# Performance work log

Hardware: AMD Instinct MI355X
Metric: run time of the kernel (lower is better)

Reference implementation:

```python
import jax, jax.numpy as jnp
import numpy as np

B, T, V, D, NOPS = 4, 2048, 8192, 512, 8
HID = 2 * D  # ActionPolicy default hidden_dim
POL_OUT = D + NOPS + D


def setup_inputs() -> dict:
    key = jax.random.key(0)
    ks = jax.random.split(key, 12)
    std = 0.02
    x = jax.random.normal(ks[0], (B, T, V), dtype=jnp.float32)
    Wc = jax.random.normal(ks[1], (D, V), dtype=jnp.float32) * std   # compress (torch Linear weight: out,in)
    We = jax.random.normal(ks[2], (V, D), dtype=jnp.float32) * std   # expand
    Wq = jax.random.normal(ks[3], (D, D), dtype=jnp.float32) * std
    Wk = jax.random.normal(ks[4], (D, D), dtype=jnp.float32) * std
    Wv = jax.random.normal(ks[5], (D, D), dtype=jnp.float32) * std
    W1 = jax.random.normal(ks[6], (HID, D), dtype=jnp.float32) * std
    b1 = jnp.zeros((HID,), dtype=jnp.float32)
    W2 = jax.random.normal(ks[7], (POL_OUT, HID), dtype=jnp.float32) * std
    b2 = jnp.zeros((POL_OUT,), dtype=jnp.float32)
    Wops = jax.random.normal(ks[8], (NOPS, D, D), dtype=jnp.float32) * std  # 8 op-bank Linears (no bias)
    decay_logit = jnp.float32(3.0)
    mem_scale = jnp.float32(0.1)
    act_scale = jnp.float32(0.1)
    return {"x": x, "Wc": Wc, "We": We, "Wq": Wq, "Wk": Wk, "Wv": Wv,
            "W1": W1, "b1": b1, "W2": W2, "b2": b2, "Wops": Wops,
            "decay_logit": decay_logit, "mem_scale": mem_scale, "act_scale": act_scale}


_ACTS = [
    lambda h: jax.nn.gelu(h, approximate=False),
    jax.nn.relu,
    lambda h: jnp.square(jax.nn.relu(h)),
    jax.nn.silu,
    jnp.tanh,
    jax.nn.sigmoid,
    lambda h: h,
    lambda h: -h,
]


def reference(x, Wc, We, Wq, Wk, Wv, W1, b1, W2, b2, Wops,
              decay_logit, mem_scale, act_scale):
    d, k = D, NOPS
    # RMSNorm over vocab dim (torch F.rms_norm, eps = dtype eps by default)
    eps = jnp.asarray(jnp.finfo(x.dtype).eps, x.dtype)
    xn = x * jax.lax.rsqrt(jnp.mean(x * x, axis=-1, keepdims=True) + eps)
    h = xn @ Wc.T                                   # (B,T,d)

    # _cross_position: causal power-decay linear attention (no softmax)
    q = h @ Wq.T
    kk = h @ Wk.T
    v = h @ Wv.T
    scores = jnp.einsum('bid,bjd->bij', q, kk)      # (B,T,T)
    pos = jnp.arange(T)
    diff = pos[None, :] - pos[:, None]              # diff[i,j] = j - i
    decay = jax.nn.sigmoid(decay_logit)
    expo = jnp.maximum(diff - 1, 0).astype(x.dtype)
    w = jnp.power(decay, expo) * (diff > 0).astype(x.dtype)
    mem = jnp.einsum('bij,bjd->bid', scores * w[None], v)
    h = h + mem_scale * mem

    # ActionPolicy MLP
    pol = jax.nn.gelu(h @ W1.T + b1, approximate=False) @ W2.T + b2
    read_w = jax.nn.softmax(pol[..., :d], axis=-1)
    op_w = jax.nn.softmax(pol[..., d:d + k], axis=-1)
    write_w = jax.nn.sigmoid(pol[..., d + k:])

    # OpBank: soft-weighted mixture of 8 Linear+activation ops
    sel = h * read_w
    hs = jnp.einsum('btd,ned->nbte', sel, Wops)     # all 8 GEMMs batched
    transformed = jnp.zeros_like(sel)
    for i, act in enumerate(_ACTS):
        transformed = transformed + op_w[..., i:i + 1] * act(hs[i])

    result = transformed * write_w
    return (result @ We.T) * act_scale              # (B,T,V)
```

## Files before the change

kernel.cpp:

```cpp
#include <hip/hip_runtime.h>
#include <cmath>


namespace {

constexpr int Tt = 2048, Vv = 8192, Dd = 512, HID = 1024, PO = 1032;
constexpr int NTOK = 8192;

typedef unsigned short u16;
typedef u16 u16x4 __attribute__((ext_vector_type(4)));
typedef u16 u16x8 __attribute__((ext_vector_type(8)));
typedef short bf16x8 __attribute__((ext_vector_type(8)));
typedef float f32x4 __attribute__((ext_vector_type(4)));

enum { EPI_STORE_F32 = 0, EPI_STORE_P, EPI_VT_P, EPI_DECAY_P, EPI_ACCUM,
       EPI_GELU_P, EPI_BIAS_F32, EPI_OUT };

__device__ __forceinline__ u16 bf16_rn(float a) {
  union { float f; unsigned u; } c; c.f = a;
  return (u16)((c.u + 0x7FFFu + ((c.u >> 16) & 1u)) >> 16);
}
__device__ __forceinline__ void split2(float a, u16& hi, u16& lo) {
  const u16 h = bf16_rn(a);
  union { unsigned u; float f; } hf; hf.u = ((unsigned)h) << 16;
  hi = h; lo = bf16_rn(a - hf.f);
}
__device__ __forceinline__ int swz(int flat, int nwg) {
  const int xcd = flat & 7, pos = flat >> 3;
  const int q8 = nwg >> 3, r8 = nwg & 7;
  return (xcd < r8 ? xcd * (q8 + 1) : r8 * (q8 + 1) + (xcd - r8) * q8) + pos;
}

template <int EPI, bool AF32, bool SKIPK, bool NGUARD>
__launch_bounds__(256, 3)
__global__ void gemm_mfma(int gridX, int N, int K,
                          const void* __restrict__ Aptr, int lda, long long sAz, long long aPlane,
                          const u16* __restrict__ Bptr, int ldb, long long sBz, long long bPlane,
                          void* __restrict__ Cptr, int ldc, long long sCz, long long cPlane,
                          const float* __restrict__ rowScale,
                          const float* __restrict__ bias,
                          const float* __restrict__ scale_ptr,
                          const float* __restrict__ decayPow) {
  const int flat = swz(blockIdx.x, gridDim.x);
  const int bx = flat % gridX, by = flat / gridX, bz = blockIdx.z;
  if (EPI == EPI_DECAY_P && bx * 64 + 63 <= by * 128) return;

  __shared__ u16 AsH[128][40], AsL[128][40], BsH[64][40], BsL[64][40];
  const int tid = threadIdx.x;
  const int sr = tid >> 1, sc = (tid & 1) << 4;
  const int br = tid >> 2, bc = (tid & 3) << 3;
  const int arow = by * 128 + sr;
  const int brow = bx * 64 + br;
  const bool bok = !NGUARD || (brow < N);
  const int w = tid >> 6, lane = tid & 63;
  const int wr = (w >> 1) << 6, wc = (w & 1) << 5;
  const int r16 = lane & 15, kg = lane >> 4;

  float ascale = 1.0f;
  if (AF32 && rowScale) ascale = rowScale[arow];

  f32x4 acc[4][2];
#pragma unroll
  for (int i = 0; i < 4; ++i)
#pragma unroll
    for (int j = 0; j < 2; ++j) acc[i][j] = (f32x4)0.0f;

  const int k0 = SKIPK ? by * 128 : 0;

  float4 raf[4];
  u16x8 rah[2], ral[2], rbh, rbl;

  auto load_tiles = [&](int kt) {
    if constexpr (AF32) {
      const float* Aq = (const float*)Aptr + (long long)bz * sAz + (long long)arow * lda + kt + sc;
#pragma unroll
      for (int u = 0; u < 4; ++u) raf[u] = *reinterpret_cast<const float4*>(Aq + 4 * u);
    } else {
      const u16* Aq = (const u16*)Aptr + (long long)bz * sAz + (long long)arow * lda + kt + sc;
      rah[0] = *reinterpret_cast<const u16x8*>(Aq);
      rah[1] = *reinterpret_cast<const u16x8*>(Aq + 8);
      ral[0] = *reinterpret_cast<const u16x8*>(Aq + aPlane);
      ral[1] = *reinterpret_cast<const u16x8*>(Aq + aPlane + 8);
    }
    if (bok) {
      const u16* Bq = Bptr + (long long)bz * sBz + (long long)brow * ldb + kt + bc;
      rbh = *reinterpret_cast<const u16x8*>(Bq);
      rbl = *reinterpret_cast<const u16x8*>(Bq + bPlane);
    } else {
      rbh = (u16x8)0; rbl = (u16x8)0;
    }
  };

  auto stage = [&]() {
    if constexpr (AF32) {
#pragma unroll
      for (int u = 0; u < 4; ++u) {
        u16 h0, h1, h2, h3, l0, l1, l2, l3;
        split2(raf[u].x * ascale, h0, l0);
        split2(raf[u].y * ascale, h1, l1);
        split2(raf[u].z * ascale, h2, l2);
        split2(raf[u].w * ascale, h3, l3);
        u16x4 hv = {h0, h1, h2, h3}, lv = {l0, l1, l2, l3};
        *reinterpret_cast<u16x4*>(&AsH[sr][sc + 4 * u]) = hv;
        *reinterpret_cast<u16x4*>(&AsL[sr][sc + 4 * u]) = lv;
      }
    } else {
      *reinterpret_cast<u16x8*>(&AsH[sr][sc]) = rah[0];
      *reinterpret_cast<u16x8*>(&AsH[sr][sc + 8]) = rah[1];
      *reinterpret_cast<u16x8*>(&AsL[sr][sc]) = ral[0];
      *reinterpret_cast<u16x8*>(&AsL[sr][sc + 8]) = ral[1];
    }
    *reinterpret_cast<u16x8*>(&BsH[br][bc]) = rbh;
    *reinterpret_cast<u16x8*>(&BsL[br][bc]) = rbl;
  };

  load_tiles(k0);
  for (int kt = k0; kt < K; kt += 32) {
    stage();
    __syncthreads();
    if (kt + 32 < K) load_tiles(kt + 32);
    bf16x8 aH[4], aL[4];
#pragma unroll
    for (int fi = 0; fi < 4; ++fi) {
      aH[fi] = *reinterpret_cast<const bf16x8*>(&AsH[wr + fi * 16 + r16][kg * 8]);
      aL[fi] = *reinterpret_cast<const bf16x8*>(&AsL[wr + fi * 16 + r16][kg * 8]);
    }
#pragma unroll
    for (int fj = 0; fj < 2; ++fj) {
      const bf16x8 bH = *reinterpret_cast<const bf16x8*>(&BsH[wc + fj * 16 + r16][kg * 8]);
      const bf16x8 bL = *reinterpret_cast<const bf16x8*>(&BsL[wc + fj * 16 + r16][kg * 8]);
#pragma unroll
      for (int fi = 0; fi < 4; ++fi) {
        acc[fi][fj] = __builtin_amdgcn_mfma_f32_16x16x32_bf16(aH[fi], bH, acc[fi][fj], 0, 0, 0);
        acc[fi][fj] = __builtin_amdgcn_mfma_f32_16x16x32_bf16(aL[fi], bH, acc[fi][fj], 0, 0, 0);
        acc[fi][fj] = __builtin_amdgcn_mfma_f32_16x16x32_bf16(aH[fi], bL, acc[fi][fj], 0, 0, 0);
      }
    }
    __syncthreads();
  }

  float scl = 1.0f;
  if (EPI == EPI_ACCUM || EPI == EPI_OUT) scl = *scale_ptr;
#pragma unroll
  for (int fi = 0; fi < 4; ++fi) {
    const int row = by * 128 + wr + fi * 16 + kg * 4;
#pragma unroll
    for (int fj = 0; fj < 2; ++fj) {
      const int col = bx * 64 + wc + fj * 16 + r16;
      if (NGUARD && col >= N) continue;
#pragma unroll
      for (int rg = 0; rg < 4; ++rg) {
        const int r = row + rg;
        float v = acc[fi][fj][rg];
        if constexpr (EPI == EPI_STORE_F32) {
          ((float*)Cptr)[(long long)bz * sCz + (long long)r * ldc + col] = v;
        } else if constexpr (EPI == EPI_STORE_P) {
          u16 hh, ll; split2(v, hh, ll);
          u16* Cp = (u16*)Cptr;
          const long long idx = (long long)bz * sCz + (long long)r * ldc + col;
          Cp[idx] = hh; Cp[idx + cPlane] = ll;
        } else if constexpr (EPI == EPI_VT_P) {
          const long long idx = (long long)(r >> 11) * ((long long)Dd * Tt) +
                                (long long)col * Tt + (r & 2047);
          u16 hh, ll; split2(v, hh, ll);
          u16* Cp = (u16*)Cptr;
          Cp[idx] = hh; Cp[idx + cPlane] = ll;
        } else if constexpr (EPI == EPI_DECAY_P) {
          const int d = col - r;
          v = (d > 0) ? v * decayPow[d - 1] : 0.0f;
          u16 hh, ll; split2(v, hh, ll);
          u16* Cp = (u16*)Cptr;
          const long long idx = (long long)bz * sCz + (long long)r * ldc + col;
          Cp[idx] = hh; Cp[idx + cPlane] = ll;
        } else if constexpr (EPI == EPI_ACCUM) {
          ((float*)Cptr)[(long long)bz * sCz + (long long)r * ldc + col] += scl * v;
        } else if constexpr (EPI == EPI_GELU_P) {
          const float t = v + bias[col];
          const float g = 0.5f * t * (1.0f + erff(t * 0.70710678118654752440f));
          u16 hh, ll; split2(g, hh, ll);
          u16* Cp = (u16*)Cptr;
          const long long idx = (long long)r * ldc + col;
          Cp[idx] = hh; Cp[idx + cPlane] = ll;
        } else if constexpr (EPI == EPI_BIAS_F32) {
          ((float*)Cptr)[(long long)r * ldc + col] = v + bias[col];
        } else {
          ((float*)Cptr)[(long long)r * ldc + col] = v * scl;
        }
      }
    }
  }
}

__launch_bounds__(256, 2)
__global__ void opbank_mfma(int gridX,
                            const u16* __restrict__ selP, long long aPlane,
                            const u16* __restrict__ WopsP, long long bPlane,
                            const float* __restrict__ opw,
                            float* __restrict__ part0, float* __restrict__ part1) {
  const int flat = swz(blockIdx.x, gridDim.x);
  const int bx = flat % gridX, by = flat / gridX, bz = blockIdx.z;
  float* __restrict__ part = (bz == 0) ? part0 : part1;

  __shared__ u16 AsH[128][40], AsL[128][40], BsH[64][40], BsL[64][40];
  const int tid = threadIdx.x;
  const int sr = tid >> 1, sc = (tid & 1) << 4;
  const int br = tid >> 2, bc = (tid & 3) << 3;
  const int arow = by * 128 + sr;
  const int brow = bx * 64 + br;
  const int w = tid >> 6, lane = tid & 63;
  const int wr = (w >> 1) << 6, wc = (w & 1) << 5;
  const int r16 = lane & 15, kg = lane >> 4;

  f32x4 res[4][2];
#pragma unroll
  for (int i = 0; i < 4; ++i)
#pragma unroll
    for (int j = 0; j < 2; ++j) res[i][j] = (f32x4)0.0f;

  u16x8 rah[2], ral[2], rbh, rbl;

  for (int nn = 0; nn < 4; ++nn) {
    const int n = bz * 4 + nn;
    const u16* Bn = WopsP + (long long)n * (Dd * Dd);
    f32x4 acc[4][2];
#pragma unroll
    for (int i = 0; i < 4; ++i)
#pragma unroll
      for (int j = 0; j < 2; ++j) acc[i][j] = (f32x4)0.0f;

    auto load_tiles = [&](int kt) {
      const u16* Aq = selP + (long long)arow * Dd + kt + sc;
      rah[0] = *reinterpret_cast<const u16x8*>(Aq);
      rah[1] = *reinterpret_cast<const u16x8*>(Aq + 8);
      ral[0] = *reinterpret_cast<const u16x8*>(Aq + aPlane);
      ral[1] = *reinterpret_cast<const u16x8*>(Aq + aPlane + 8);
      const u16* Bq = Bn + (long long)brow * Dd + kt + bc;
      rbh = *reinterpret_cast<const u16x8*>(Bq);
      rbl = *reinterpret_cast<const u16x8*>(Bq + bPlane);
    };
    load_tiles(0);
    for (int kt = 0; kt < Dd; kt += 32) {
      *reinterpret_cast<u16x8*>(&AsH[sr][sc]) = rah[0];
      *reinterpret_cast<u16x8*>(&AsH[sr][sc + 8]) = rah[1];
      *reinterpret_cast<u16x8*>(&AsL[sr][sc]) = ral[0];
      *reinterpret_cast<u16x8*>(&AsL[sr][sc + 8]) = ral[1];
      *reinterpret_cast<u16x8*>(&BsH[br][bc]) = rbh;
      *reinterpret_cast<u16x8*>(&BsL[br][bc]) = rbl;
      __syncthreads();
      if (kt + 32 < Dd) load_tiles(kt + 32);
      bf16x8 aH[4], aL[4];
#pragma unroll
      for (int fi = 0; fi < 4; ++fi) {
        aH[fi] = *reinterpret_cast<const bf16x8*>(&AsH[wr + fi * 16 + r16][kg * 8]);
        aL[fi] = *reinterpret_cast<const bf16x8*>(&AsL[wr + fi * 16 + r16][kg * 8]);
      }
#pragma unroll
      for (int fj = 0; fj < 2; ++fj) {
        const bf16x8 bH = *reinterpret_cast<const bf16x8*>(&BsH[wc + fj * 16 + r16][kg * 8]);
        const bf16x8 bL = *reinterpret_cast<const bf16x8*>(&BsL[wc + fj * 16 + r16][kg * 8]);
#pragma unroll
        for (int fi = 0; fi < 4; ++fi) {
          acc[fi][fj] = __builtin_amdgcn_mfma_f32_16x16x32_bf16(aH[fi], bH, acc[fi][fj], 0, 0, 0);
          acc[fi][fj] = __builtin_amdgcn_mfma_f32_16x16x32_bf16(aL[fi], bH, acc[fi][fj], 0, 0, 0);
          acc[fi][fj] = __builtin_amdgcn_mfma_f32_16x16x32_bf16(aH[fi], bL, acc[fi][fj], 0, 0, 0);
        }
      }
      __syncthreads();
    }
#pragma unroll
    for (int fi = 0; fi < 4; ++fi) {
#pragma unroll
      for (int rg = 0; rg < 4; ++rg) {
        const int r = by * 128 + wr + fi * 16 + kg * 4 + rg;
        const float ow = opw[(long long)r * 8 + n];
#pragma unroll
        for (int fj = 0; fj < 2; ++fj) {
          const float hv = acc[fi][fj][rg];
          float av;
          switch (n) {
            case 0: av = 0.5f * hv * (1.0f + erff(hv * 0.70710678118654752440f)); break;
            case 1: av = fmaxf(hv, 0.0f); break;
            case 2: { const float r_ = fmaxf(hv, 0.0f); av = r_ * r_; } break;
            case 3: av = hv / (1.0f + expf(-hv)); break;
            case 4: av = tanhf(hv); break;
            case 5: av = 1.0f / (1.0f + expf(-hv)); break;
            case 6: av = hv; break;
            default: av = -hv; break;
          }
          res[fi][fj][rg] += ow * av;
        }
      }
    }
  }
#pragma unroll
  for (int fi = 0; fi < 4; ++fi)
#pragma unroll
    for (int fj = 0; fj < 2; ++fj) {
      const int col = bx * 64 + wc + fj * 16 + r16;
#pragma unroll
      for (int rg = 0; rg < 4; ++rg) {
        const int r = by * 128 + wr + fi * 16 + kg * 4 + rg;
        part[(long long)r * Dd + col] = res[fi][fj][rg];
      }
    }
}

__global__ void decaypow_kernel(const float* __restrict__ decay_logit,
                                float* __restrict__ pw) {
  const int e = blockIdx.x * 256 + threadIdx.x;
  if (e < Tt) {
    const float decay = 1.0f / (1.0f + expf(-*decay_logit));
    pw[e] = powf(decay, (float)e);
  }
}

__global__ void rmsnorm_kernel(const float* __restrict__ x,
                               float* __restrict__ rstd) {
  const int t = blockIdx.x, tid = threadIdx.x;
  const float4* xr = reinterpret_cast<const float4*>(x + (long long)t * Vv);
  float s = 0.0f;
  for (int i = tid; i < Vv / 4; i += 256) {
    const float4 v = xr[i];
    s += v.x * v.x + v.y * v.y + v.z * v.z + v.w * v.w;
  }
  __shared__ float red[256];
  red[tid] = s;
  __syncthreads();
  for (int st = 128; st > 0; st >>= 1) {
    if (tid < st) red[tid] += red[tid + st];
    __syncthreads();
  }
  if (tid == 0) rstd[t] = rsqrtf(red[0] / (float)Vv + 1.1920929e-07f);
}

__global__ void split_kernel(const float* __restrict__ src, u16* __restrict__ dst,
                             long long n) {
  const long long i0 = ((long long)blockIdx.x * 256 + threadIdx.x) * 4;
  const long long stride = (long long)gridDim.x * 1024;
  for (long long i = i0; i < n; i += stride) {
    const float4 v = *reinterpret_cast<const float4*>(src + i);
    u16 hh, ll; u16x4 hv, lv;
    split2(v.x, hh, ll); hv[0] = hh; lv[0] = ll;
    split2(v.y, hh, ll); hv[1] = hh; lv[1] = ll;
    split2(v.z, hh, ll); hv[2] = hh; lv[2] = ll;
    split2(v.w, hh, ll); hv[3] = hh; lv[3] = ll;
    *reinterpret_cast<u16x4*>(&dst[i]) = hv;
    *reinterpret_cast<u16x4*>(&dst[n + i]) = lv;
  }
}

__global__ void policy_kernel(float* __restrict__ pol, const float* __restrict__ h,
                              u16* __restrict__ selP, float* __restrict__ opw) {
  const int t = blockIdx.x, tid = threadIdx.x;
  float* prow = pol + (long long)t * PO;
  __shared__ float red[256];
  const float v0 = prow[tid], v1 = prow[tid + 256];
  red[tid] = fmaxf(v0, v1);
  __syncthreads();
  for (int s = 128; s > 0; s >>= 1) {
    if (tid < s) red[tid] = fmaxf(red[tid], red[tid + s]);
    __syncthreads();
  }
  const float mx = red[0];
  __syncthreads();
  const float e0 = expf(v0 - mx), e1 = expf(v1 - mx);
  red[tid] = e0 + e1;
  __syncthreads();
  for (int s = 128; s > 0; s >>= 1) {
    if (tid < s) red[tid] += red[tid + s];
    __syncthreads();
  }
  const float inv = 1.0f / red[0];
  const float* hrow = h + (long long)t * Dd;
  u16 hh, ll;
  const float s0 = hrow[tid] * e0 * inv;
  split2(s0, hh, ll);
  selP[(long long)t * Dd + tid] = hh;
  selP[(long long)t * Dd + tid + 4194304] = ll;
  const float s1 = hrow[tid + 256] * e1 * inv;
  split2(s1, hh, ll);
  selP[(long long)t * Dd + tid + 256] = hh;
  selP[(long long)t * Dd + tid + 256 + 4194304] = ll;
  if (tid == 0) {
    float ov[8];
    float om = -1e30f;
    for (int n = 0; n < 8; ++n) { ov[n] = prow[512 + n]; om = fmaxf(om, ov[n]); }
    float osum = 0.0f;
    for (int n = 0; n < 8; ++n) { ov[n] = expf(ov[n] - om); osum += ov[n]; }
    const float oi = 1.0f / osum;
    for (int n = 0; n < 8; ++n) opw[(long long)t * 8 + n] = ov[n] * oi;
  }
  const float w0 = prow[520 + tid];
  prow[520 + tid] = 1.0f / (1.0f + expf(-w0));
  const float w1 = prow[520 + 256 + tid];
  prow[520 + 256 + tid] = 1.0f / (1.0f + expf(-w1));
}

__global__ void combine_kernel(const float* __restrict__ p0, const float* __restrict__ p1,
                               const float* __restrict__ pol, u16* __restrict__ resP) {
  const long long total = (long long)NTOK * Dd;
  const long long i0 = ((long long)blockIdx.x * 256 + threadIdx.x) * 4;
  const long long stride = (long long)gridDim.x * 1024;
  for (long long i = i0; i < total; i += stride) {
    const float4 a = *reinterpret_cast<const float4*>(p0 + i);
    const float4 b = *reinterpret_cast<const float4*>(p1 + i);
    const long long t = i >> 9;
    const int e = (int)(i & 511);
    const float4 wv = *reinterpret_cast<const float4*>(pol + t * PO + 520 + e);
    u16 hh, ll; u16x4 hv, lv;
    split2((a.x + b.x) * wv.x, hh, ll); hv[0] = hh; lv[0] = ll;
    split2((a.y + b.y) * wv.y, hh, ll); hv[1] = hh; lv[1] = ll;
    split2((a.z + b.z) * wv.z, hh, ll); hv[2] = hh; lv[2] = ll;
    split2((a.w + b.w) * wv.w, hh, ll); hv[3] = hh; lv[3] = ll;
    *reinterpret_cast<u16x4*>(&resP[i]) = hv;
    *reinterpret_cast<u16x4*>(&resP[i + 4194304]) = lv;
  }
}

}

extern "C" void kernel_launch(void* const* d_in, const int* in_sizes, int n_in,
                              void* d_out, int out_size, void* d_ws, size_t ws_size,
                              hipStream_t stream) {
  const float* x    = (const float*)d_in[0];
  const float* Wc   = (const float*)d_in[1];
  const float* We   = (const float*)d_in[2];
  const float* Wq   = (const float*)d_in[3];
  const float* Wk   = (const float*)d_in[4];
  const float* Wv   = (const float*)d_in[5];
  const float* W1   = (const float*)d_in[6];
  const float* b1   = (const float*)d_in[7];
  const float* W2   = (const float*)d_in[8];
  const float* b2   = (const float*)d_in[9];
  const float* Wops = (const float*)d_in[10];
  const float* dlg  = (const float*)d_in[11];
  const float* msc  = (const float*)d_in[12];
  const float* asc  = (const float*)d_in[13];

  float* ws = (float*)d_ws;
  float* h    = ws;
  u16*   qkP  = (u16*)(ws + 4194304);
  u16*   vTP  = (u16*)(ws + 12582912);
  u16*   scP  = (u16*)(ws + 16777216);
  float* pol  = ws + 25165824;
  float* rstd = ws + 33619968;
  float* dpw  = rstd + 8192;
  float* opw  = dpw + 2048;
  float* out  = (float*)d_out;

  u16*   WcP   = scP;
  u16*   WqP   = (u16*)(ws + 20971520);
  u16*   W1P   = (u16*)(ws + 25165824);
  u16*   W2P   = (u16*)(ws + 12582912);
  u16*   WopsP = (u16*)(ws + 16777216);
  u16*   a1P   = (u16*)(ws + 16777216);
  u16*   selP  = qkP;
  u16*   resP  = (u16*)(ws + 8388608);
  u16*   WeP   = qkP;
  float* p0    = h;
  float* p1    = ws + 12582912;

  decaypow_kernel<<<8, 256, 0, stream>>>(dlg, dpw);
  rmsnorm_kernel<<<NTOK, 256, 0, stream>>>(x, rstd);
  split_kernel<<<2048, 256, 0, stream>>>(Wc, WcP, 4194304LL);
  split_kernel<<<256, 256, 0, stream>>>(Wq, WqP, 262144LL);
  split_kernel<<<256, 256, 0, stream>>>(Wk, WqP + 524288, 262144LL);
  split_kernel<<<256, 256, 0, stream>>>(Wv, WqP + 1048576, 262144LL);

  gemm_mfma<EPI_STORE_F32, true, false, false><<<dim3(512, 1, 1), 256, 0, stream>>>(
      8, Dd, Vv, x, Vv, 0, 0, WcP, Vv, 0, 4194304, h, Dd, 0, 0,
      rstd, nullptr, nullptr, nullptr);
  gemm_mfma<EPI_STORE_P, true, false, false><<<dim3(512, 1, 2), 256, 0, stream>>>(
      8, Dd, Dd, h, Dd, 0, 0, WqP, Dd, 524288, 262144, qkP, Dd, 8388608, 4194304,
      nullptr, nullptr, nullptr, nullptr);
  gemm_mfma<EPI_VT_P, true, false, false><<<dim3(512, 1, 1), 256, 0, stream>>>(
      8, Dd, Dd, h, Dd, 0, 0, WqP + 1048576, Dd, 0, 262144, vTP, 0, 0, 4194304,
      nullptr, nullptr, nullptr, nullptr);
  gemm_mfma<EPI_DECAY_P, false, false, false><<<dim3(512, 1, 4), 256, 0, stream>>>(
      32, Tt, Dd, qkP, Dd, 1048576, 4194304, qkP + 8388608, Dd, 1048576, 4194304,
      scP, Tt, 4194304, 16777216, nullptr, nullptr, nullptr, dpw);
  gemm_mfma<EPI_ACCUM, false, true, false><<<dim3(128, 1, 4), 256, 0, stream>>>(
      8, Dd, Tt, scP, Tt, 4194304, 16777216, vTP, Tt, 1048576, 4194304,
      h, Dd, 1048576, 0, nullptr, nullptr, msc, nullptr);
  split_kernel<<<512, 256, 0, stream>>>(W1, W1P, 524288LL);
  gemm_mfma<EPI_GELU_P, true, false, false><<<dim3(1024, 1, 1), 256, 0, stream>>>(
      16, HID, Dd, h, Dd, 0, 0, W1P, Dd, 0, 524288, a1P, HID, 0, 8388608,
      nullptr, b1, nullptr, nullptr);
  split_kernel<<<1024, 256, 0, stream>>>(W2, W2P, 1056768LL);
  gemm_mfma<EPI_BIAS_F32, false, false, true><<<dim3(1088, 1, 1), 256, 0, stream>>>(
      17, PO, HID, a1P, HID, 0, 8388608, W2P, HID, 0, 1056768, pol, PO, 0, 0,
      nullptr, b2, nullptr, nullptr);
  policy_kernel<<<NTOK, 256, 0, stream>>>(pol, h, selP, opw);
  split_kernel<<<2048, 256, 0, stream>>>(Wops, WopsP, 2097152LL);
  opbank_mfma<<<dim3(512, 1, 2), 256, 0, stream>>>(
      8, selP, 4194304, WopsP, 2097152, opw, p0, p1);
  split_kernel<<<2048, 256, 0, stream>>>(We, WeP, 4194304LL);
  combine_kernel<<<2048, 256, 0, stream>>>(p0, p1, pol, resP);
  gemm_mfma<EPI_OUT, false, false, false><<<dim3(8192, 1, 1), 256, 0, stream>>>(
      128, Vv, Dd, resP, Dd, 0, 4194304, WeP, Dd, 0, 4194304, out, Vv, 0, 0,
      nullptr, nullptr, asc, nullptr);
}
```

Baseline: 1.680 ms.

## Split-K the compress GEMM, relayout LDS tiles by k-slice, raise occupancy

The x@Wc compress GEMM (K=8192, only 512 blocks) is split into four K-chunks across blockIdx.z. Each chunk writes partials to separate workspace buffers, and a new combine4 kernel sums them. Shared-memory tiles are reorganized from padded row-major [row][40] into [kslice][row][8], so fragment loads are contiguous per k-group. Launch bounds go from 3 to 4 waves per SIMD, and the row-scale multiply is gated by a new template flag. The cost is an extra pass over the partial sums, possible LDS bank conflicts from the unpadded layout, and register pressure at the higher occupancy.

```diff
diff --git a/kernel.cpp b/kernel.cpp
--- a/kernel.cpp
+++ b/kernel.cpp
@@ -31,8 +31,8 @@
   return (xcd < r8 ? xcd * (q8 + 1) : r8 * (q8 + 1) + (xcd - r8) * q8) + pos;
 }
 
-template <int EPI, bool AF32, bool SKIPK, bool NGUARD>
-__launch_bounds__(256, 3)
+template <int EPI, bool AF32, bool RS, bool SKIPK, bool NGUARD>
+__launch_bounds__(256, 4)
 __global__ void gemm_mfma(int gridX, int N, int K,
                           const void* __restrict__ Aptr, int lda, long long sAz, long long aPlane,
                           const u16* __restrict__ Bptr, int ldb, long long sBz, long long bPlane,
@@ -45,10 +45,10 @@
   const int bx = flat % gridX, by = flat / gridX, bz = blockIdx.z;
   if (EPI == EPI_DECAY_P && bx * 64 + 63 <= by * 128) return;
 
-  __shared__ u16 AsH[128][40], AsL[128][40], BsH[64][40], BsL[64][40];
+  __shared__ u16 AsH[4][128][8], AsL[4][128][8], BsH[4][64][8], BsL[4][64][8];
   const int tid = threadIdx.x;
-  const int sr = tid >> 1, sc = (tid & 1) << 4;
-  const int br = tid >> 2, bc = (tid & 3) << 3;
+  const int sr = tid >> 1, ss = tid & 1;
+  const int br = tid >> 2, sbc = tid & 3;
   const int arow = by * 128 + sr;
   const int brow = bx * 64 + br;
   const bool bok = !NGUARD || (brow < N);
@@ -57,7 +57,7 @@
   const int r16 = lane & 15, kg = lane >> 4;
 
   float ascale = 1.0f;
-  if (AF32 && rowScale) ascale = rowScale[arow];
+  if (RS) ascale = rowScale[arow];
 
   f32x4 acc[4][2];
 #pragma unroll
@@ -72,18 +72,18 @@
 
   auto load_tiles = [&](int kt) {
     if constexpr (AF32) {
-      const float* Aq = (const float*)Aptr + (long long)bz * sAz + (long long)arow * lda + kt + sc;
+      const float* Aq = (const float*)Aptr + (long long)bz * sAz + (long long)arow * lda + kt + 16 * ss;
 #pragma unroll
       for (int u = 0; u < 4; ++u) raf[u] = *reinterpret_cast<const float4*>(Aq + 4 * u);
     } else {
-      const u16* Aq = (const u16*)Aptr + (long long)bz * sAz + (long long)arow * lda + kt + sc;
+      const u16* Aq = (const u16*)Aptr + (long long)bz * sAz + (long long)arow * lda + kt + 16 * ss;
       rah[0] = *reinterpret_cast<const u16x8*>(Aq);
       rah[1] = *reinterpret_cast<const u16x8*>(Aq + 8);
       ral[0] = *reinterpret_cast<const u16x8*>(Aq + aPlane);
       ral[1] = *reinterpret_cast<const u16x8*>(Aq + aPlane + 8);
     }
     if (bok) {
-      const u16* Bq = Bptr + (long long)bz * sBz + (long long)brow * ldb + kt + bc;
+      const u16* Bq = Bptr + (long long)bz * sBz + (long long)brow * ldb + kt + 8 * sbc;
       rbh = *reinterpret_cast<const u16x8*>(Bq);
       rbl = *reinterpret_cast<const u16x8*>(Bq + bPlane);
     } else {
@@ -94,24 +94,30 @@
   auto stage = [&]() {
     if constexpr (AF32) {
 #pragma unroll
-      for (int u = 0; u < 4; ++u) {
-        u16 h0, h1, h2, h3, l0, l1, l2, l3;
-        split2(raf[u].x * ascale, h0, l0);
-        split2(raf[u].y * ascale, h1, l1);
-        split2(raf[u].z * ascale, h2, l2);
-        split2(raf[u].w * ascale, h3, l3);
-        u16x4 hv = {h0, h1, h2, h3}, lv = {l0, l1, l2, l3};
-        *reinterpret_cast<u16x4*>(&AsH[sr][sc + 4 * u]) = hv;
-        *reinterpret_cast<u16x4*>(&AsL[sr][sc + 4 * u]) = lv;
+      for (int half = 0; half < 2; ++half) {
+        u16x8 hv, lv;
+#pragma unroll
+        for (int u = 0; u < 2; ++u) {
+          const float4 f = raf[half * 2 + u];
+          u16 hh, ll;
+          float x0 = f.x, x1 = f.y, x2 = f.z, x3 = f.w;
+          if (RS) { x0 *= ascale; x1 *= ascale; x2 *= ascale; x3 *= ascale; }
+          split2(x0, hh, ll); hv[4 * u + 0] = hh; lv[4 * u + 0] = ll;
+          split2(x1, hh, ll); hv[4 * u + 1] = hh; lv[4 * u + 1] = ll;
+          split2(x2, hh, ll); hv[4 * u + 2] = hh; lv[4 * u + 2] = ll;
+          split2(x3, hh, ll); hv[4 * u + 3] = hh; lv[4 * u + 3] = ll;
+        }
+        *reinterpret_cast<u16x8*>(&AsH[2 * ss + half][sr][0]) = hv;
+        *reinterpret_cast<u16x8*>(&AsL[2 * ss + half][sr][0]) = lv;
       }
     } else {
-      *reinterpret_cast<u16x8*>(&AsH[sr][sc]) = rah[0];
-      *reinterpret_cast<u16x8*>(&AsH[sr][sc + 8]) = rah[1];
-      *reinterpret_cast<u16x8*>(&AsL[sr][sc]) = ral[0];
-      *reinterpret_cast<u16x8*>(&AsL[sr][sc + 8]) = ral[1];
-    }
-    *reinterpret_cast<u16x8*>(&BsH[br][bc]) = rbh;
-    *reinterpret_cast<u16x8*>(&BsL[br][bc]) = rbl;
+      *reinterpret_cast<u16x8*>(&AsH[2 * ss][sr][0]) = rah[0];
+      *reinterpret_cast<u16x8*>(&AsH[2 * ss + 1][sr][0]) = rah[1];
+      *reinterpret_cast<u16x8*>(&AsL[2 * ss][sr][0]) = ral[0];
+      *reinterpret_cast<u16x8*>(&AsL[2 * ss + 1][sr][0]) = ral[1];
+    }
+    *reinterpret_cast<u16x8*>(&BsH[sbc][br][0]) = rbh;
+    *reinterpret_cast<u16x8*>(&BsL[sbc][br][0]) = rbl;
   };
 
   load_tiles(k0);
@@ -122,13 +128,13 @@
     bf16x8 aH[4], aL[4];
 #pragma unroll
     for (int fi = 0; fi < 4; ++fi) {
-      aH[fi] = *reinterpret_cast<const bf16x8*>(&AsH[wr + fi * 16 + r16][kg * 8]);
-      aL[fi] = *reinterpret_cast<const bf16x8*>(&AsL[wr + fi * 16 + r16][kg * 8]);
+      aH[fi] = *reinterpret_cast<const bf16x8*>(&AsH[kg][wr + fi * 16 + r16][0]);
+      aL[fi] = *reinterpret_cast<const bf16x8*>(&AsL[kg][wr + fi * 16 + r16][0]);
     }
 #pragma unroll
     for (int fj = 0; fj < 2; ++fj) {
-      const bf16x8 bH = *reinterpret_cast<const bf16x8*>(&BsH[wc + fj * 16 + r16][kg * 8]);
-      const bf16x8 bL = *reinterpret_cast<const bf16x8*>(&BsL[wc + fj * 16 + r16][kg * 8]);
+      const bf16x8 bH = *reinterpret_cast<const bf16x8*>(&BsH[kg][wc + fj * 16 + r16][0]);
+      const bf16x8 bL = *reinterpret_cast<const bf16x8*>(&BsL[kg][wc + fj * 16 + r16][0]);
 #pragma unroll
       for (int fi = 0; fi < 4; ++fi) {
         acc[fi][fj] = __builtin_amdgcn_mfma_f32_16x16x32_bf16(aH[fi], bH, acc[fi][fj], 0, 0, 0);
@@ -201,10 +207,10 @@
   const int bx = flat % gridX, by = flat / gridX, bz = blockIdx.z;
   float* __restrict__ part = (bz == 0) ? part0 : part1;
 
-  __shared__ u16 AsH[128][40], AsL[128][40], BsH[64][40], BsL[64][40];
+  __shared__ u16 AsH[4][128][8], AsL[4][128][8], BsH[4][64][8], BsL[4][64][8];
   const int tid = threadIdx.x;
-  const int sr = tid >> 1, sc = (tid & 1) << 4;
-  const int br = tid >> 2, bc = (tid & 3) << 3;
+  const int sr = tid >> 1, ss = tid & 1;
+  const int br = tid >> 2, sbc = tid & 3;
   const int arow = by * 128 + sr;
   const int brow = bx * 64 + br;
   const int w = tid >> 6, lane = tid & 63;
@@ -229,35 +235,35 @@
       for (int j = 0; j < 2; ++j) acc[i][j] = (f32x4)0.0f;
 
     auto load_tiles = [&](int kt) {
-      const u16* Aq = selP + (long long)arow * Dd + kt + sc;
+      const u16* Aq = selP + (long long)arow * Dd + kt + 16 * ss;
       rah[0] = *reinterpret_cast<const u16x8*>(Aq);
       rah[1] = *reinterpret_cast<const u16x8*>(Aq + 8);
       ral[0] = *reinterpret_cast<const u16x8*>(Aq + aPlane);
       ral[1] = *reinterpret_cast<const u16x8*>(Aq + aPlane + 8);
-      const u16* Bq = Bn + (long long)brow * Dd + kt + bc;
+      const u16* Bq = Bn + (long long)brow * Dd + kt + 8 * sbc;
       rbh = *reinterpret_cast<const u16x8*>(Bq);
       rbl = *reinterpret_cast<const u16x8*>(Bq + bPlane);
     };
     load_tiles(0);
     for (int kt = 0; kt < Dd; kt += 32) {
-      *reinterpret_cast<u16x8*>(&AsH[sr][sc]) = rah[0];
-      *reinterpret_cast<u16x8*>(&AsH[sr][sc + 8]) = rah[1];
-      *reinterpret_cast<u16x8*>(&AsL[sr][sc]) = ral[0];
-      *reinterpret_cast<u16x8*>(&AsL[sr][sc + 8]) = ral[1];
-      *reinterpret_cast<u16x8*>(&BsH[br][bc]) = rbh;
-      *reinterpret_cast<u16x8*>(&BsL[br][bc]) = rbl;
+      *reinterpret_cast<u16x8*>(&AsH[2 * ss][sr][0]) = rah[0];
+      *reinterpret_cast<u16x8*>(&AsH[2 * ss + 1][sr][0]) = rah[1];
+      *reinterpret_cast<u16x8*>(&AsL[2 * ss][sr][0]) = ral[0];
+      *reinterpret_cast<u16x8*>(&AsL[2 * ss + 1][sr][0]) = ral[1];
+      *reinterpret_cast<u16x8*>(&BsH[sbc][br][0]) = rbh;
+      *reinterpret_cast<u16x8*>(&BsL[sbc][br][0]) = rbl;
       __syncthreads();
       if (kt + 32 < Dd) load_tiles(kt + 32);
       bf16x8 aH[4], aL[4];
 #pragma unroll
       for (int fi = 0; fi < 4; ++fi) {
-        aH[fi] = *reinterpret_cast<const bf16x8*>(&AsH[wr + fi * 16 + r16][kg * 8]);
-        aL[fi] = *reinterpret_cast<const bf16x8*>(&AsL[wr + fi * 16 + r16][kg * 8]);
+        aH[fi] = *reinterpret_cast<const bf16x8*>(&AsH[kg][wr + fi * 16 + r16][0]);
+        aL[fi] = *reinterpret_cast<const bf16x8*>(&AsL[kg][wr + fi * 16 + r16][0]);
       }
 #pragma unroll
       for (int fj = 0; fj < 2; ++fj) {
-        const bf16x8 bH = *reinterpret_cast<const bf16x8*>(&BsH[wc + fj * 16 + r16][kg * 8]);
-        const bf16x8 bL = *reinterpret_cast<const bf16x8*>(&BsL[wc + fj * 16 + r16][kg * 8]);
+        const bf16x8 bH = *reinterpret_cast<const bf16x8*>(&BsH[kg][wc + fj * 16 + r16][0]);
+        const bf16x8 bL = *reinterpret_cast<const bf16x8*>(&BsL[kg][wc + fj * 16 + r16][0]);
 #pragma unroll
         for (int fi = 0; fi < 4; ++fi) {
           acc[fi][fj] = __builtin_amdgcn_mfma_f32_16x16x32_bf16(aH[fi], bH, acc[fi][fj], 0, 0, 0);
@@ -346,6 +352,25 @@
     split2(v.w, hh, ll); hv[3] = hh; lv[3] = ll;
     *reinterpret_cast<u16x4*>(&dst[i]) = hv;
     *reinterpret_cast<u16x4*>(&dst[n + i]) = lv;
+  }
+}
+
+__global__ void combine4_kernel(float* __restrict__ h, const float* __restrict__ p1,
+                                const float* __restrict__ p2, const float* __restrict__ p3) {
+  const long long total = (long long)NTOK * Dd;
+  const long long i0 = ((long long)blockIdx.x * 256 + threadIdx.x) * 4;
+  const long long stride = (long long)gridDim.x * 1024;
+  for (long long i = i0; i < total; i += stride) {
+    const float4 a = *reinterpret_cast<const float4*>(h + i);
+    const float4 b = *reinterpret_cast<const float4*>(p1 + i);
+    const float4 c = *reinterpret_cast<const float4*>(p2 + i);
+    const float4 d = *reinterpret_cast<const float4*>(p3 + i);
+    float4 o;
+    o.x = a.x + b.x + c.x + d.x;
+    o.y = a.y + b.y + c.y + d.y;
+    o.z = a.z + b.z + c.z + d.z;
+    o.w = a.w + b.w + c.w + d.w;
+    *reinterpret_cast<float4*>(h + i) = o;
   }
 }
 
@@ -457,8 +482,11 @@
   u16*   selP  = qkP;
   u16*   resP  = (u16*)(ws + 8388608);
   u16*   WeP   = qkP;
-  float* p0    = h;
-  float* p1    = ws + 12582912;
+  float* ob0   = h;
+  float* ob1   = ws + 12582912;
+  float* sk1   = ws + 4194304;
+  float* sk2   = ws + 8388608;
+  float* sk3   = ws + 12582912;
 
   decaypow_kernel<<<8, 256, 0, stream>>>(dlg, dpw);
   rmsnorm_kernel<<<NTOK, 256, 0, stream>>>(x, rstd);
@@ -467,36 +495,37 @@
   split_kernel<<<256, 256, 0, stream>>>(Wk, WqP + 524288, 262144LL);
   split_kernel<<<256, 256, 0, stream>>>(Wv, WqP + 1048576, 262144LL);
 
-  gemm_mfma<EPI_STORE_F32, true, false, false><<<dim3(512, 1, 1), 256, 0, stream>>>(
-      8, Dd, Vv, x, Vv, 0, 0, WcP, Vv, 0, 4194304, h, Dd, 0, 0,
+  gemm_mfma<EPI_STORE_F32, true, true, false, false><<<dim3(512, 1, 4), 256, 0, stream>>>(
+      8, Dd, 2048, x, Vv, 2048, 0, WcP, Vv, 2048, 4194304, h, Dd, 4194304, 0,
       rstd, nullptr, nullptr, nullptr);
-  gemm_mfma<EPI_STORE_P, true, false, false><<<dim3(512, 1, 2), 256, 0, stream>>>(
+  combine4_kernel<<<2048, 256, 0, stream>>>(h, sk1, sk2, sk3);
+  gemm_mfma<EPI_STORE_P, true, false, false, false><<<dim3(512, 1, 2), 256, 0, stream>>>(
       8, Dd, Dd, h, Dd, 0, 0, WqP, Dd, 524288, 262144, qkP, Dd, 8388608, 4194304,
       nullptr, nullptr, nullptr, nullptr);
-  gemm_mfma<EPI_VT_P, true, false, false><<<dim3(512, 1, 1), 256, 0, stream>>>(
+  gemm_mfma<EPI_VT_P, true, false, false, false><<<dim3(512, 1, 1), 256, 0, stream>>>(
       8, Dd, Dd, h, Dd, 0, 0, WqP + 1048576, Dd, 0, 262144, vTP, 0, 0, 4194304,
       nullptr, nullptr, nullptr, nullptr);
-  gemm_mfma<EPI_DECAY_P, false, false, false><<<dim3(512, 1, 4), 256, 0, stream>>>(
+  gemm_mfma<EPI_DECAY_P, false, false, false, false><<<dim3(512, 1, 4), 256, 0, stream>>>(
       32, Tt, Dd, qkP, Dd, 1048576, 4194304, qkP + 8388608, Dd, 1048576, 4194304,
       scP, Tt, 4194304, 16777216, nullptr, nullptr, nullptr, dpw);
-  gemm_mfma<EPI_ACCUM, false, true, false><<<dim3(128, 1, 4), 256, 0, stream>>>(
+  gemm_mfma<EPI_ACCUM, false, false, true, false><<<dim3(128, 1, 4), 256, 0, stream>>>(
       8, Dd, Tt, scP, Tt, 4194304, 16777216, vTP, Tt, 1048576, 4194304,
       h, Dd, 1048576, 0, nullptr, nullptr, msc, nullptr);
   split_kernel<<<512, 256, 0, stream>>>(W1, W1P, 524288LL);
-  gemm_mfma<EPI_GELU_P, true, false, false><<<dim3(1024, 1, 1), 256, 0, stream>>>(
+  gemm_mfma<EPI_GELU_P, true, false, false, false><<<dim3(1024, 1, 1), 256, 0, stream>>>(
       16, HID, Dd, h, Dd, 0, 0, W1P, Dd, 0, 524288, a1P, HID, 0, 8388608,
       nullptr, b1, nullptr, nullptr);
   split_kernel<<<1024, 256, 0, stream>>>(W2, W2P, 1056768LL);
-  gemm_mfma<EPI_BIAS_F32, false, false, true><<<dim3(1088, 1, 1), 256, 0, stream>>>(
+  gemm_mfma<EPI_BIAS_F32, false, false, false, true><<<dim3(1088, 1, 1), 256, 0, stream>>>(
       17, PO, HID, a1P, HID, 0, 8388608, W2P, HID, 0, 1056768, pol, PO, 0, 0,
       nullptr, b2, nullptr, nullptr);
   policy_kernel<<<NTOK, 256, 0, stream>>>(pol, h, selP, opw);
   split_kernel<<<2048, 256, 0, stream>>>(Wops, WopsP, 2097152LL);
   opbank_mfma<<<dim3(512, 1, 2), 256, 0, stream>>>(
-      8, selP, 4194304, WopsP, 2097152, opw, p0, p1);
+      8, selP, 4194304, WopsP, 2097152, opw, ob0, ob1);
   split_kernel<<<2048, 256, 0, stream>>>(We, WeP, 4194304LL);
-  combine_kernel<<<2048, 256, 0, stream>>>(p0, p1, pol, resP);
-  gemm_mfma<EPI_OUT, false, false, false><<<dim3(8192, 1, 1), 256, 0, stream>>>(
+  combine_kernel<<<2048, 256, 0, stream>>>(ob0, ob1, pol, resP);
+  gemm_mfma<EPI_OUT, false, false, false, false><<<dim3(8192, 1, 1), 256, 0, stream>>>(
       128, Vv, Dd, resP, Dd, 0, 4194304, WeP, Dd, 0, 4194304, out, Vv, 0, 0,
       nullptr, nullptr, asc, nullptr);
 }
```

Result: faster. 1.574 ms (-6.3%).
